# Performance work log

Hardware: AMD Instinct MI355X
Metric: run time of the kernel (lower is better)

Reference implementation:

```python
import jax, jax.numpy as jnp
import numpy as np

N_NODES = 100000
N_EDGES = 1600000
IN_CH, HID_CH, OUT_CH = 128, 128, 64


def setup_inputs() -> dict:
    key = jax.random.key(0)
    k_x, k_e, k1, k2, k3 = jax.random.split(key, 5)
    x = jax.random.normal(k_x, (N_NODES, IN_CH), dtype=jnp.float32)
    edge_index = jax.random.randint(k_e, (2, N_EDGES), 0, N_NODES, dtype=jnp.int64)
    # Glorot-ish init for the three GCNConv weight matrices (no bias).
    W1 = jax.random.normal(k1, (IN_CH, HID_CH), dtype=jnp.float32) / np.sqrt(IN_CH)
    W2 = jax.random.normal(k2, (HID_CH, HID_CH), dtype=jnp.float32) / np.sqrt(HID_CH)
    W3 = jax.random.normal(k3, (HID_CH, OUT_CH), dtype=jnp.float32) / np.sqrt(HID_CH)
    return {"x": x, "edge_index": edge_index, "W1": W1, "W2": W2, "W3": W3}


def _gcn_layer(x, src, dst, W):
    # GCNConv(normalize=False, bias=False): transform then sum-aggregate over edges.
    h = x @ W                      # [N, d_out]
    msgs = h[src]                  # [E, d_out] gather from source nodes
    return jax.ops.segment_sum(msgs, dst, num_segments=N_NODES)  # scatter-add to targets


def reference(x, edge_index, W1, W2, W3):
    src, dst = edge_index[0], edge_index[1]  # PyG flow: source_to_target
    h = _gcn_layer(x, src, dst, W1)
    h = _gcn_layer(h, src, dst, W2)
    h = _gcn_layer(h, src, dst, W3)
    return h  # [N, OUT_CH]
```

## Files before the change

kernel.cpp:

```cpp
#include <hip/hip_runtime.h>

#define N_NODES 100000
#define N_EDGES 1600000
#define CAP 48
#define NBUCK 256
#define NPB 391
#define SCAP 8192
#define EPB 4096
#define NBIN ((N_EDGES + EPB - 1) / EPB)

typedef unsigned int uint;
typedef unsigned short ushort;

__device__ __forceinline__ void fma4(float4& c, float s, const float4& w) {
    c.x += s * w.x; c.y += s * w.y; c.z += s * w.z; c.w += s * w.w;
}

__device__ __forceinline__ ushort bf16r(float f) {
    union { float f; uint u; } v; v.f = f;
    return (ushort)((v.u + 0x7fffu + ((v.u >> 16) & 1u)) >> 16);
}

struct alignas(16) GemmSmem {
    float Xs[128][36];
    float Ws[32][64];
};

template <typename OutT>
__device__ __forceinline__ void gemm64_block(GemmSmem& sm, int bid,
                                             const float* __restrict__ X,
                                             const float* __restrict__ W,
                                             OutT* __restrict__ H, int n) {
    const int tid  = threadIdx.x;
    const int row0 = bid * 128;
    const int rg   = tid >> 4;
    const int cg   = tid & 15;

    float4 acc0[8];
#pragma unroll
    for (int r = 0; r < 8; r++) acc0[r] = make_float4(0.f, 0.f, 0.f, 0.f);

    const int lr = tid >> 1;
    const int lh = tid & 1;
    int grow = row0 + lr; if (grow > n - 1) grow = n - 1;
    const float* gx_base = X + (size_t)grow * 128 + lh * 16;

    for (int k0 = 0; k0 < 128; k0 += 32) {
        const float* gx = gx_base + k0;
#pragma unroll
        for (int i = 0; i < 4; i++)
            *(float4*)&sm.Xs[lr][lh * 16 + 4 * i] = *(const float4*)(gx + 4 * i);
        const float4* gw = (const float4*)(W + (size_t)k0 * 64);
        float4* sw = (float4*)&sm.Ws[0][0];
#pragma unroll
        for (int i = 0; i < 2; i++) sw[tid + 256 * i] = gw[tid + 256 * i];
        __syncthreads();

#pragma unroll
        for (int kk = 0; kk < 32; kk += 4) {
            float4 w00 = *(const float4*)&sm.Ws[kk + 0][cg * 4];
            float4 w01 = *(const float4*)&sm.Ws[kk + 1][cg * 4];
            float4 w02 = *(const float4*)&sm.Ws[kk + 2][cg * 4];
            float4 w03 = *(const float4*)&sm.Ws[kk + 3][cg * 4];
#pragma unroll
            for (int r = 0; r < 8; r++) {
                float4 a = *(const float4*)&sm.Xs[rg * 8 + r][kk];
                fma4(acc0[r], a.x, w00);
                fma4(acc0[r], a.y, w01);
                fma4(acc0[r], a.z, w02);
                fma4(acc0[r], a.w, w03);
            }
        }
        __syncthreads();
    }

#pragma unroll
    for (int r = 0; r < 8; r++) {
        int row = row0 + rg * 8 + r;
        if (row < n) {
            if constexpr (sizeof(OutT) == 2) {
                ushort4 o0 = make_ushort4(bf16r(acc0[r].x), bf16r(acc0[r].y),
                                          bf16r(acc0[r].z), bf16r(acc0[r].w));
                *(ushort4*)&H[(size_t)row * 64 + cg * 4] = o0;
            } else {
                *(float4*)&H[(size_t)row * 64 + cg * 4] = *(float4*)&acc0[r];
            }
        }
    }
}

union BinWcSmem {
    struct { int ecnt[NBUCK]; int base[NBUCK]; int lcur[NBUCK]; } b;
    GemmSmem g;
};

__global__ void __launch_bounds__(256) bin_wc(const int* __restrict__ src,
                                              const int* __restrict__ dst,
                                              int* __restrict__ gcur,
                                              uint2* __restrict__ seg, int E,
                                              const float* __restrict__ W1,
                                              const float* __restrict__ W2,
                                              const float* __restrict__ W3,
                                              float* __restrict__ W23,
                                              float* __restrict__ Wc) {
    __shared__ BinWcSmem sh;
    if (blockIdx.x == gridDim.x - 1) {
        gemm64_block<float>(sh.g, 0, W2, W3, W23, 128);
        __syncthreads();
        gemm64_block<float>(sh.g, 0, W1, W23, Wc, 128);
        return;
    }
    const int t = threadIdx.x;
    sh.b.ecnt[t] = 0; sh.b.lcur[t] = 0;
    __syncthreads();
    const int e0 = blockIdx.x * EPB;
#pragma unroll
    for (int k = 0; k < EPB / 256; k++) {
        int i = e0 + k * 256 + t;
        if (i < E) atomicAdd(&sh.b.ecnt[dst[i] / NPB], 1);
    }
    __syncthreads();
    sh.b.base[t] = (sh.b.ecnt[t] > 0) ? atomicAdd(&gcur[t], sh.b.ecnt[t]) : 0;
    __syncthreads();
#pragma unroll
    for (int k = 0; k < EPB / 256; k++) {
        int i = e0 + k * 256 + t;
        if (i < E) {
            int d = dst[i];
            int b = d / NPB;
            int s = sh.b.base[b] + atomicAdd(&sh.b.lcur[b], 1);
            if (s < SCAP) seg[(size_t)b * SCAP + s] = make_uint2((uint)src[i], (uint)d);
        }
    }
}

union CsrGemmSmem {
    int lc[NPB];
    GemmSmem g;
};

__global__ void __launch_bounds__(256, 3) csr_gemm(const int* __restrict__ gcur,
                                                   const uint2* __restrict__ seg,
                                                   int* __restrict__ col,
                                                   int* __restrict__ cnt,
                                                   const float* __restrict__ X,
                                                   const float* __restrict__ Wc,
                                                   ushort* __restrict__ Y, int n) {
    __shared__ CsrGemmSmem sh;
    if (blockIdx.x < NBUCK) {
        const int b = blockIdx.x;
        const int t = threadIdx.x;
        for (int i = t; i < NPB; i += 256) sh.lc[i] = 0;
        __syncthreads();
        int m = gcur[b]; if (m > SCAP) m = SCAP;
        const uint2* sg = seg + (size_t)b * SCAP;
        const int node0 = b * NPB;
        for (int i = t; i < m; i += 256) {
            uint2 e = sg[i];
            int d = (int)e.y;
            int slot = atomicAdd(&sh.lc[d - node0], 1);
            if (slot < CAP) col[(size_t)d * CAP + slot] = (int)e.x;
        }
        __syncthreads();
        for (int i = t; i < NPB; i += 256) {
            int node = node0 + i;
            if (node < n) cnt[node] = (sh.lc[i] > CAP) ? CAP : sh.lc[i];
        }
    } else {
        gemm64_block<ushort>(sh.g, blockIdx.x - NBUCK, X, Wc, Y, n);
    }
}

__device__ __forceinline__ float2 bf2f(uint u) {
    union { uint u; float f; } a, b;
    a.u = u << 16; b.u = u & 0xffff0000u;
    return make_float2(a.f, b.f);
}

template <bool FINAL>
__global__ void __launch_bounds__(256) agg64(const uint4* __restrict__ T_in,
                                             const int* __restrict__ cnt,
                                             const int* __restrict__ col,
                                             void* __restrict__ T_out, int n) {
    int gid  = blockIdx.x * blockDim.x + threadIdx.x;
    int node = gid >> 3;
    int lane = gid & 7;
    if (node >= n) return;
    int m = cnt[node]; if (m > CAP) m = CAP;
    const int* cb = col + (size_t)node * CAP;
    const uint4* tb = T_in + lane;
    float4 accA = make_float4(0.f, 0.f, 0.f, 0.f);
    float4 accB = make_float4(0.f, 0.f, 0.f, 0.f);
    int j = 0;
    for (; j + 8 <= m; j += 8) {
        int4 c0 = *(const int4*)&cb[j];
        int4 c1 = *(const int4*)&cb[j + 4];
        uint4 u0 = tb[(size_t)c0.x * 8];
        uint4 u1 = tb[(size_t)c0.y * 8];
        uint4 u2 = tb[(size_t)c0.z * 8];
        uint4 u3 = tb[(size_t)c0.w * 8];
        uint4 u4 = tb[(size_t)c1.x * 8];
        uint4 u5 = tb[(size_t)c1.y * 8];
        uint4 u6 = tb[(size_t)c1.z * 8];
        uint4 u7 = tb[(size_t)c1.w * 8];
        float2 p0 = bf2f(u0.x), p1 = bf2f(u1.x), p2 = bf2f(u2.x), p3 = bf2f(u3.x);
        float2 p4 = bf2f(u4.x), p5 = bf2f(u5.x), p6 = bf2f(u6.x), p7 = bf2f(u7.x);
        accA.x += ((p0.x + p1.x) + (p2.x + p3.x)) + ((p4.x + p5.x) + (p6.x + p7.x));
        accA.y += ((p0.y + p1.y) + (p2.y + p3.y)) + ((p4.y + p5.y) + (p6.y + p7.y));
        float2 q0 = bf2f(u0.y), q1 = bf2f(u1.y), q2 = bf2f(u2.y), q3 = bf2f(u3.y);
        float2 q4 = bf2f(u4.y), q5 = bf2f(u5.y), q6 = bf2f(u6.y), q7 = bf2f(u7.y);
        accA.z += ((q0.x + q1.x) + (q2.x + q3.x)) + ((q4.x + q5.x) + (q6.x + q7.x));
        accA.w += ((q0.y + q1.y) + (q2.y + q3.y)) + ((q4.y + q5.y) + (q6.y + q7.y));
        float2 r0 = bf2f(u0.z), r1 = bf2f(u1.z), r2 = bf2f(u2.z), r3 = bf2f(u3.z);
        float2 r4 = bf2f(u4.z), r5 = bf2f(u5.z), r6 = bf2f(u6.z), r7 = bf2f(u7.z);
        accB.x += ((r0.x + r1.x) + (r2.x + r3.x)) + ((r4.x + r5.x) + (r6.x + r7.x));
        accB.y += ((r0.y + r1.y) + (r2.y + r3.y)) + ((r4.y + r5.y) + (r6.y + r7.y));
        float2 s0 = bf2f(u0.w), s1 = bf2f(u1.w), s2 = bf2f(u2.w), s3 = bf2f(u3.w);
        float2 s4 = bf2f(u4.w), s5 = bf2f(u5.w), s6 = bf2f(u6.w), s7 = bf2f(u7.w);
        accB.z += ((s0.x + s1.x) + (s2.x + s3.x)) + ((s4.x + s5.x) + (s6.x + s7.x));
        accB.w += ((s0.y + s1.y) + (s2.y + s3.y)) + ((s4.y + s5.y) + (s6.y + s7.y));
    }
    for (; j + 4 <= m; j += 4) {
        int4 c0 = *(const int4*)&cb[j];
        uint4 u0 = tb[(size_t)c0.x * 8];
        uint4 u1 = tb[(size_t)c0.y * 8];
        uint4 u2 = tb[(size_t)c0.z * 8];
        uint4 u3 = tb[(size_t)c0.w * 8];
        float2 p0 = bf2f(u0.x), p1 = bf2f(u1.x), p2 = bf2f(u2.x), p3 = bf2f(u3.x);
        accA.x += (p0.x + p1.x) + (p2.x + p3.x);
        accA.y += (p0.y + p1.y) + (p2.y + p3.y);
        float2 q0 = bf2f(u0.y), q1 = bf2f(u1.y), q2 = bf2f(u2.y), q3 = bf2f(u3.y);
        accA.z += (q0.x + q1.x) + (q2.x + q3.x);
        accA.w += (q0.y + q1.y) + (q2.y + q3.y);
        float2 r0 = bf2f(u0.z), r1 = bf2f(u1.z), r2 = bf2f(u2.z), r3 = bf2f(u3.z);
        accB.x += (r0.x + r1.x) + (r2.x + r3.x);
        accB.y += (r0.y + r1.y) + (r2.y + r3.y);
        float2 s0 = bf2f(u0.w), s1 = bf2f(u1.w), s2 = bf2f(u2.w), s3 = bf2f(u3.w);
        accB.z += (s0.x + s1.x) + (s2.x + s3.x);
        accB.w += (s0.y + s1.y) + (s2.y + s3.y);
    }
    for (; j < m; j++) {
        uint4 u = tb[(size_t)cb[j] * 8];
        float2 p = bf2f(u.x), q = bf2f(u.y), r = bf2f(u.z), s = bf2f(u.w);
        accA.x += p.x; accA.y += p.y; accA.z += q.x; accA.w += q.y;
        accB.x += r.x; accB.y += r.y; accB.z += s.x; accB.w += s.y;
    }
    if (FINAL) {
        ((float4*)T_out)[(size_t)node * 16 + lane * 2]     = accA;
        ((float4*)T_out)[(size_t)node * 16 + lane * 2 + 1] = accB;
    } else {
        uint4 o;
        o.x = (uint)bf16r(accA.x) | ((uint)bf16r(accA.y) << 16);
        o.y = (uint)bf16r(accA.z) | ((uint)bf16r(accA.w) << 16);
        o.z = (uint)bf16r(accB.x) | ((uint)bf16r(accB.y) << 16);
        o.w = (uint)bf16r(accB.z) | ((uint)bf16r(accB.w) << 16);
        ((uint4*)T_out)[(size_t)node * 8 + lane] = o;
    }
}


static inline size_t align_up(size_t x, size_t a) { return (x + a - 1) & ~(a - 1); }

extern "C" void kernel_launch(void* const* d_in, const int* in_sizes, int n_in,
                              void* d_out, int out_size, void* d_ws, size_t ws_size,
                              hipStream_t stream) {
    const float* x  = (const float*)d_in[0];
    const int*   ei = (const int*)d_in[1];
    const float* W1 = (const float*)d_in[2];
    const float* W2 = (const float*)d_in[3];
    const float* W3 = (const float*)d_in[4];
    float* out = (float*)d_out;

    const int N = N_NODES;
    const int E = N_EDGES;
    const int* src = ei;
    const int* dst = ei + E;

    char* p = (char*)d_ws;
    int*    gcur = (int*)p;   p += align_up((size_t)NBUCK * 4, 256);
    int*    cnt  = (int*)p;   p += align_up((size_t)N * 4, 256);
    uint2*  seg  = (uint2*)p; p += align_up((size_t)NBUCK * SCAP * 8, 256);
    int*    col  = (int*)p;   p += align_up((size_t)N * CAP * 4, 256);
    float*  W23  = (float*)p; p += align_up((size_t)128 * 64 * 4, 256);
    float*  Wc   = (float*)p; p += align_up((size_t)128 * 64 * 4, 256);
    ushort* Y    = (ushort*)p; p += align_up((size_t)N * 64 * 2, 256);
    ushort* Za   = (ushort*)p; p += align_up((size_t)N * 64 * 2, 256);

    hipMemsetAsync(gcur, 0, (size_t)NBUCK * 4, stream);

    bin_wc<<<NBIN + 1, 256, 0, stream>>>(src, dst, gcur, seg, E,
                                         W1, W2, W3, W23, Wc);

    const int gemm_blocks = (N + 127) / 128;
    csr_gemm<<<NBUCK + gemm_blocks, 256, 0, stream>>>(gcur, seg, col, cnt,
                                                      x, Wc, Y, N);

    const int agg_blocks = (N * 8 + 255) / 256;
    agg64<false><<<agg_blocks, 256, 0, stream>>>((const uint4*)Y,  cnt, col, Za, N);
    agg64<false><<<agg_blocks, 256, 0, stream>>>((const uint4*)Za, cnt, col, Y,  N);
    agg64<true ><<<agg_blocks, 256, 0, stream>>>((const uint4*)Y,  cnt, col, out, N);
}
```

Baseline: 254.7 us.

## Enlarge X@Wc GEMM tile to 256 rows and reuse local slots in binning

The main X@Wc GEMM now uses 256-row tiles. Each thread computes 8 rows by 8 columns, so every shared-memory X read feeds twice as many FMAs, and half as many blocks are launched. The binning kernel keeps src/dst and the shared-atomic slot from the counting pass in registers. This removes the second global read of the edges and the second round of shared atomics. The costs are higher register pressure and a larger shared-memory footprint (about 45 KB), which may lower occupancy under launch_bounds(256,3).

Result: slower. 262.0 us (+2.9%).

```diff
diff --git a/kernel.cpp b/kernel.cpp
--- a/kernel.cpp
+++ b/kernel.cpp
@@ -21,30 +21,25 @@
     return (ushort)((v.u + 0x7fffu + ((v.u >> 16) & 1u)) >> 16);
 }
 
-struct alignas(16) GemmSmem {
+struct alignas(16) GemmSmemS {
     float Xs[128][36];
     float Ws[32][64];
 };
 
-template <typename OutT>
-__device__ __forceinline__ void gemm64_block(GemmSmem& sm, int bid,
-                                             const float* __restrict__ X,
-                                             const float* __restrict__ W,
-                                             OutT* __restrict__ H, int n) {
+__device__ __forceinline__ void gemm128_block(GemmSmemS& sm,
+                                              const float* __restrict__ X,
+                                              const float* __restrict__ W,
+                                              float* __restrict__ H, int n) {
     const int tid  = threadIdx.x;
-    const int row0 = bid * 128;
     const int rg   = tid >> 4;
     const int cg   = tid & 15;
-
     float4 acc0[8];
 #pragma unroll
     for (int r = 0; r < 8; r++) acc0[r] = make_float4(0.f, 0.f, 0.f, 0.f);
-
     const int lr = tid >> 1;
     const int lh = tid & 1;
-    int grow = row0 + lr; if (grow > n - 1) grow = n - 1;
+    int grow = lr; if (grow > n - 1) grow = n - 1;
     const float* gx_base = X + (size_t)grow * 128 + lh * 16;
-
     for (int k0 = 0; k0 < 128; k0 += 32) {
         const float* gx = gx_base + k0;
 #pragma unroll
@@ -55,7 +50,6 @@
 #pragma unroll
         for (int i = 0; i < 2; i++) sw[tid + 256 * i] = gw[tid + 256 * i];
         __syncthreads();
-
 #pragma unroll
         for (int kk = 0; kk < 32; kk += 4) {
             float4 w00 = *(const float4*)&sm.Ws[kk + 0][cg * 4];
@@ -73,25 +67,87 @@
         }
         __syncthreads();
     }
+#pragma unroll
+    for (int r = 0; r < 8; r++) {
+        int row = rg * 8 + r;
+        if (row < n) *(float4*)&H[(size_t)row * 64 + cg * 4] = *(float4*)&acc0[r];
+    }
+}
+
+struct alignas(16) GemmSmemL {
+    float Xs[256][36];
+    float Ws[32][64];
+};
+
+__device__ __forceinline__ void gemm256_block(GemmSmemL& sm, int bid,
+                                              const float* __restrict__ X,
+                                              const float* __restrict__ W,
+                                              ushort* __restrict__ H, int n) {
+    const int tid  = threadIdx.x;
+    const int row0 = bid * 256;
+    const int rg   = tid >> 3;
+    const int cg   = tid & 7;
+
+    float4 accA[8], accB[8];
+#pragma unroll
+    for (int r = 0; r < 8; r++) {
+        accA[r] = make_float4(0.f, 0.f, 0.f, 0.f);
+        accB[r] = make_float4(0.f, 0.f, 0.f, 0.f);
+    }
+
+    int grow = row0 + tid; if (grow > n - 1) grow = n - 1;
+    const float* gx_base = X + (size_t)grow * 128;
+
+    for (int k0 = 0; k0 < 128; k0 += 32) {
+        const float* gx = gx_base + k0;
+#pragma unroll
+        for (int i = 0; i < 8; i++)
+            *(float4*)&sm.Xs[tid][4 * i] = *(const float4*)(gx + 4 * i);
+        const float4* gw = (const float4*)(W + (size_t)k0 * 64);
+        float4* sw = (float4*)&sm.Ws[0][0];
+#pragma unroll
+        for (int i = 0; i < 2; i++) sw[tid + 256 * i] = gw[tid + 256 * i];
+        __syncthreads();
+
+#pragma unroll
+        for (int kk = 0; kk < 32; kk += 4) {
+            float4 w0a = *(const float4*)&sm.Ws[kk + 0][cg * 8];
+            float4 w0b = *(const float4*)&sm.Ws[kk + 0][cg * 8 + 4];
+            float4 w1a = *(const float4*)&sm.Ws[kk + 1][cg * 8];
+            float4 w1b = *(const float4*)&sm.Ws[kk + 1][cg * 8 + 4];
+            float4 w2a = *(const float4*)&sm.Ws[kk + 2][cg * 8];
+            float4 w2b = *(const float4*)&sm.Ws[kk + 2][cg * 8 + 4];
+            float4 w3a = *(const float4*)&sm.Ws[kk + 3][cg * 8];
+            float4 w3b = *(const float4*)&sm.Ws[kk + 3][cg * 8 + 4];
+#pragma unroll
+            for (int r = 0; r < 8; r++) {
+                float4 a = *(const float4*)&sm.Xs[rg * 8 + r][kk];
+                fma4(accA[r], a.x, w0a); fma4(accB[r], a.x, w0b);
+                fma4(accA[r], a.y, w1a); fma4(accB[r], a.y, w1b);
+                fma4(accA[r], a.z, w2a); fma4(accB[r], a.z, w2b);
+                fma4(accA[r], a.w, w3a); fma4(accB[r], a.w, w3b);
+            }
+        }
+        __syncthreads();
+    }
 
 #pragma unroll
     for (int r = 0; r < 8; r++) {
         int row = row0 + rg * 8 + r;
         if (row < n) {
-            if constexpr (sizeof(OutT) == 2) {
-                ushort4 o0 = make_ushort4(bf16r(acc0[r].x), bf16r(acc0[r].y),
-                                          bf16r(acc0[r].z), bf16r(acc0[r].w));
-                *(ushort4*)&H[(size_t)row * 64 + cg * 4] = o0;
-            } else {
-                *(float4*)&H[(size_t)row * 64 + cg * 4] = *(float4*)&acc0[r];
-            }
+            ushort4 oA = make_ushort4(bf16r(accA[r].x), bf16r(accA[r].y),
+                                      bf16r(accA[r].z), bf16r(accA[r].w));
+            ushort4 oB = make_ushort4(bf16r(accB[r].x), bf16r(accB[r].y),
+                                      bf16r(accB[r].z), bf16r(accB[r].w));
+            *(ushort4*)&H[(size_t)row * 64 + cg * 8]     = oA;
+            *(ushort4*)&H[(size_t)row * 64 + cg * 8 + 4] = oB;
         }
     }
 }
 
 union BinWcSmem {
-    struct { int ecnt[NBUCK]; int base[NBUCK]; int lcur[NBUCK]; } b;
-    GemmSmem g;
+    struct { int ecnt[NBUCK]; int base[NBUCK]; } b;
+    GemmSmemS g;
 };
 
 __global__ void __launch_bounds__(256) bin_wc(const int* __restrict__ src,
@@ -105,38 +161,46 @@
                                               float* __restrict__ Wc) {
     __shared__ BinWcSmem sh;
     if (blockIdx.x == gridDim.x - 1) {
-        gemm64_block<float>(sh.g, 0, W2, W3, W23, 128);
-        __syncthreads();
-        gemm64_block<float>(sh.g, 0, W1, W23, Wc, 128);
+        gemm128_block(sh.g, W2, W3, W23, 128);
+        __syncthreads();
+        gemm128_block(sh.g, W1, W23, Wc, 128);
         return;
     }
     const int t = threadIdx.x;
-    sh.b.ecnt[t] = 0; sh.b.lcur[t] = 0;
+    sh.b.ecnt[t] = 0;
     __syncthreads();
     const int e0 = blockIdx.x * EPB;
-#pragma unroll
-    for (int k = 0; k < EPB / 256; k++) {
-        int i = e0 + k * 256 + t;
-        if (i < E) atomicAdd(&sh.b.ecnt[dst[i] / NPB], 1);
-    }
-    __syncthreads();
-    sh.b.base[t] = (sh.b.ecnt[t] > 0) ? atomicAdd(&gcur[t], sh.b.ecnt[t]) : 0;
-    __syncthreads();
+    uint sreg[EPB / 256];
+    int  dreg[EPB / 256];
+    int  slreg[EPB / 256];
 #pragma unroll
     for (int k = 0; k < EPB / 256; k++) {
         int i = e0 + k * 256 + t;
         if (i < E) {
             int d = dst[i];
+            sreg[k] = (uint)src[i];
+            dreg[k] = d;
+            slreg[k] = atomicAdd(&sh.b.ecnt[d / NPB], 1);
+        }
+    }
+    __syncthreads();
+    sh.b.base[t] = (sh.b.ecnt[t] > 0) ? atomicAdd(&gcur[t], sh.b.ecnt[t]) : 0;
+    __syncthreads();
+#pragma unroll
+    for (int k = 0; k < EPB / 256; k++) {
+        int i = e0 + k * 256 + t;
+        if (i < E) {
+            int d = dreg[k];
             int b = d / NPB;
-            int s = sh.b.base[b] + atomicAdd(&sh.b.lcur[b], 1);
-            if (s < SCAP) seg[(size_t)b * SCAP + s] = make_uint2((uint)src[i], (uint)d);
+            int s = sh.b.base[b] + slreg[k];
+            if (s < SCAP) seg[(size_t)b * SCAP + s] = make_uint2(sreg[k], (uint)d);
         }
     }
 }
 
 union CsrGemmSmem {
     int lc[NPB];
-    GemmSmem g;
+    GemmSmemL g;
 };
 
 __global__ void __launch_bounds__(256, 3) csr_gemm(const int* __restrict__ gcur,
@@ -167,7 +231,7 @@
             if (node < n) cnt[node] = (sh.lc[i] > CAP) ? CAP : sh.lc[i];
         }
     } else {
-        gemm64_block<ushort>(sh.g, blockIdx.x - NBUCK, X, Wc, Y, n);
+        gemm256_block(sh.g, blockIdx.x - NBUCK, X, Wc, Y, n);
     }
 }
 
@@ -291,7 +355,7 @@
     bin_wc<<<NBIN + 1, 256, 0, stream>>>(src, dst, gcur, seg, E,
                                          W1, W2, W3, W23, Wc);
 
-    const int gemm_blocks = (N + 127) / 128;
+    const int gemm_blocks = (N + 255) / 256;
     csr_gemm<<<NBUCK + gemm_blocks, 256, 0, stream>>>(gcur, seg, col, cnt,
                                                       x, Wc, Y, N);
 
```

## Stage binned edges in shared memory to coalesce bucket writes

Applied to the files above, without the earlier changes.

The binning kernel now reads src and dst once into registers and takes per-edge local slots from the first counting atomic, which removes the second pass over global memory and the second atomic round. It scans the bucket counts in LDS, scatters the edges into a bucket-sorted staging buffer in shared memory, then writes them out in order so that consecutive threads write contiguous runs of each bucket's segment. The cost is a 32KB LDS staging buffer per block, which may reduce occupancy, plus extra barriers for the scan.

Result: no change. 252.7 us (-0.8%).

```diff
diff --git a/kernel.cpp b/kernel.cpp
--- a/kernel.cpp
+++ b/kernel.cpp
@@ -90,7 +90,12 @@
 }
 
 union BinWcSmem {
-    struct { int ecnt[NBUCK]; int base[NBUCK]; int lcur[NBUCK]; } b;
+    struct {
+        int ecnt[NBUCK];
+        int base[NBUCK];
+        int lofs[NBUCK];
+        uint2 estage[EPB];
+    } b;
     GemmSmem g;
 };
 
@@ -111,26 +116,54 @@
         return;
     }
     const int t = threadIdx.x;
-    sh.b.ecnt[t] = 0; sh.b.lcur[t] = 0;
+    sh.b.ecnt[t] = 0;
     __syncthreads();
     const int e0 = blockIdx.x * EPB;
-#pragma unroll
-    for (int k = 0; k < EPB / 256; k++) {
-        int i = e0 + k * 256 + t;
-        if (i < E) atomicAdd(&sh.b.ecnt[dst[i] / NPB], 1);
-    }
-    __syncthreads();
-    sh.b.base[t] = (sh.b.ecnt[t] > 0) ? atomicAdd(&gcur[t], sh.b.ecnt[t]) : 0;
-    __syncthreads();
+    uint sreg[EPB / 256];
+    int  dreg[EPB / 256];
+    int  slreg[EPB / 256];
 #pragma unroll
     for (int k = 0; k < EPB / 256; k++) {
         int i = e0 + k * 256 + t;
         if (i < E) {
             int d = dst[i];
-            int b = d / NPB;
-            int s = sh.b.base[b] + atomicAdd(&sh.b.lcur[b], 1);
-            if (s < SCAP) seg[(size_t)b * SCAP + s] = make_uint2((uint)src[i], (uint)d);
-        }
+            sreg[k] = (uint)src[i];
+            dreg[k] = d;
+            slreg[k] = atomicAdd(&sh.b.ecnt[d / NPB], 1);
+        }
+    }
+    __syncthreads();
+    const int c = sh.b.ecnt[t];
+    sh.b.base[t] = (c > 0) ? atomicAdd(&gcur[t], c) : 0;
+    sh.b.lofs[t] = c;
+    __syncthreads();
+#pragma unroll
+    for (int off = 1; off < NBUCK; off <<= 1) {
+        int u = (t >= off) ? sh.b.lofs[t - off] : 0;
+        __syncthreads();
+        sh.b.lofs[t] += u;
+        __syncthreads();
+    }
+    const int excl = sh.b.lofs[t] - c;
+    __syncthreads();
+    sh.b.lofs[t] = excl;
+    __syncthreads();
+#pragma unroll
+    for (int k = 0; k < EPB / 256; k++) {
+        int i = e0 + k * 256 + t;
+        if (i < E) {
+            int b = dreg[k] / NPB;
+            sh.b.estage[sh.b.lofs[b] + slreg[k]] =
+                make_uint2(sreg[k], (uint)dreg[k]);
+        }
+    }
+    __syncthreads();
+    const int total = min(E - e0, EPB);
+    for (int i = t; i < total; i += 256) {
+        uint2 e = sh.b.estage[i];
+        int b = (int)e.y / NPB;
+        int s = sh.b.base[b] + (i - sh.b.lofs[b]);
+        if (s < SCAP) seg[(size_t)b * SCAP + s] = e;
     }
 }
 
```
